# Kernel tuning notes

Measured on AMD Instinct MI355X. Metric: run time of the kernel, lower is better.

The kernel has to match this reference:

```python
import jax, jax.numpy as jnp
import numpy as np

OBS, N, IN, H = 15, 50000, 2, 64
GX, GY = 4, 4
NS = 4.0


def setup_inputs() -> dict:
    key = jax.random.key(0)
    ks = jax.random.split(key, 15)
    tgt = jax.random.uniform(ks[0], (OBS, 1, IN), minval=-2.0, maxval=2.0, dtype=jnp.float32)
    oth = jax.random.uniform(ks[1], (OBS, N, IN), minval=-3.0, maxval=3.0, dtype=jnp.float32)
    mask = jax.random.randint(ks[2], (OBS, N), 0, 2, dtype=jnp.int32)
    s = 1.0 / np.sqrt(H)
    u = lambda k, shp: jax.random.uniform(k, shp, minval=-s, maxval=s, dtype=jnp.float32)
    return dict(
        observed_trajectory_target=tgt,
        observed_trajectory_others=oth,
        neighbor_mask=mask,
        W_ih=u(ks[3], (4 * H, IN)), b_ih=u(ks[4], (4 * H,)),
        W_hh=u(ks[5], (4 * H, H)), b_hh=u(ks[6], (4 * H,)),
        W1=u(ks[7], (H, H * GX * GY)), b1=u(ks[8], (H,)),
        W2=u(ks[9], (H, H)), b2=u(ks[10], (H,)),
        Wc=u(ks[11], (2, H)), bc=u(ks[12], (2,)),
    )


def reference(observed_trajectory_target, observed_trajectory_others, neighbor_mask,
              W_ih, b_ih, W_hh, b_hh, W1, b1, W2, b2, Wc, bc):
    cw = NS / GX   # cell width
    ch = NS / GY   # cell height
    hx, hy = GX // 2, GY // 2
    half = NS / 2.0

    def lstm_cell(x, h, c):
        # torch LSTMCell: gates ordered i, f, g, o
        gates = x @ W_ih.T + b_ih + h @ W_hh.T + b_hh
        i, f, g, o = jnp.split(gates, 4, axis=-1)
        c_new = jax.nn.sigmoid(f) * c + jax.nn.sigmoid(i) * jnp.tanh(g)
        h_new = jax.nn.sigmoid(o) * jnp.tanh(c_new)
        return h_new, c_new

    def step(carry, xs):
        h_t, c_t, h_o, c_o, _ = carry
        xt, xo, m = xs                      # xt: [2], xo: [N,2], m: [N]
        ref_pos = xt[:2]
        h_t, c_t = lstm_cell(xt[None, :], h_t, c_t)
        h_o, c_o = lstm_cell(xo, h_o, c_o)
        # social grid binning (dropout is identity in eval mode)
        rel = xo[:, :2] - ref_pos           # [N,2]
        within = (jnp.abs(rel[:, 0]) <= half) & (jnp.abs(rel[:, 1]) <= half)
        cx = jnp.trunc(rel[:, 0] / cw).astype(jnp.int32) + hx  # trunc == torch .long()
        cy = jnp.trunc(rel[:, 1] / ch).astype(jnp.int32) + hy
        valid = within & (cx >= 0) & (cx < GX) & (cy >= 0) & (cy < GY) & (m != 0)
        idx = jnp.where(valid, cy * GX + cx, 0)
        contrib = jnp.where(valid[:, None], h_o, 0.0)
        social = jax.ops.segment_sum(contrib, idx, num_segments=GX * GY)  # [16,H]
        sv = social.reshape(1, -1)          # [1, 16*H]
        ctx = jax.nn.relu(sv @ W1.T + b1) @ W2.T + b2
        combined = h_t + ctx
        return (h_t, c_t, h_o, c_o, combined), None

    Nn = observed_trajectory_others.shape[1]
    init = (jnp.zeros((1, H), jnp.float32), jnp.zeros((1, H), jnp.float32),
            jnp.zeros((Nn, H), jnp.float32), jnp.zeros((Nn, H), jnp.float32),
            jnp.zeros((1, H), jnp.float32))
    xs = (observed_trajectory_target[:, 0, :], observed_trajectory_others, neighbor_mask)
    (h_t, c_t, h_o, c_o, combined), _ = jax.lax.scan(step, init, xs)
    return combined @ Wc.T + bc  # [1, 2]
```

## Files before the change

### kernel.cpp

```cpp
#include <hip/hip_runtime.h>
#include <stdint.h>

#define OBS 15
#define NTOT 50000
#define HDIM 64
#define NPB 16

typedef __attribute__((ext_vector_type(8))) short short8;
typedef __attribute__((ext_vector_type(4))) float f32x4;

static __device__ __forceinline__ unsigned short f2bf(float f) {
  unsigned u = __float_as_uint(f);
  u += 0x7fff + ((u >> 16) & 1);
  return (unsigned short)(u >> 16);
}
static __device__ __forceinline__ float bf2f(unsigned short b) {
  return __uint_as_float(((unsigned)b) << 16);
}

#if __has_builtin(__builtin_amdgcn_exp2f)
#define EXP2F(x) __builtin_amdgcn_exp2f(x)
#else
#define EXP2F(x) exp2f(x)
#endif
#if __has_builtin(__builtin_amdgcn_rcpf)
#define RCPF(x) __builtin_amdgcn_rcpf(x)
#else
#define RCPF(x) (1.0f / (x))
#endif

static __device__ __forceinline__ float sigm(float x) {
  return RCPF(1.0f + EXP2F(-1.4426950408889634f * x));
}
static __device__ __forceinline__ float tanh_(float x) {
  return 2.0f * RCPF(1.0f + EXP2F(-2.8853900817779268f * x)) - 1.0f;
}

static __device__ __forceinline__ int hidx(int r, int cb) {
  return r * 64 + ((cb ^ (r & 7)) << 3);
}

__global__ void k_zero(float* social) {
  social[threadIdx.x] = 0.0f;
}

#define MFMA_BF16 __builtin_amdgcn_mfma_f32_16x16x32_bf16

__global__ __launch_bounds__(256, 2)
void k_neigh(
    const float* __restrict__ tgt,
    const float* __restrict__ oth,
    const int* __restrict__ mask,
    const float* __restrict__ W_ih,
    const float* __restrict__ b_ih,
    const float* __restrict__ W_hh,
    const float* __restrict__ b_hh,
    float* __restrict__ social)
{
  __shared__ __align__(16) unsigned short h2[2][NPB][HDIM];
  __shared__ float xs[OBS][NPB][2];

  const int tid = threadIdx.x;
  const int l = tid & 63;
  const int w = tid >> 6;
  const int t15 = l & 15;
  const int g4 = l >> 4;
  const int n0 = blockIdx.x * NPB;

  for (int i = tid; i < OBS * NPB * 2; i += 256) {
    ((float*)xs)[i] = oth[(i >> 5) * (NTOT * 2) + n0 * 2 + (i & 31)];
  }
  for (int i = tid; i < NPB * HDIM / 2; i += 256) ((unsigned int*)h2[0])[i] = 0u;

  short8 Bhi0, Bhi1, Bhi2, Bhi3, Bhi4, Bhi5, Bhi6, Bhi7;
  short8 Blo0, Blo1, Blo2, Blo3, Blo4, Blo5, Blo6, Blo7;
  float bias2[4], wih0[4], wih1[4];
#define LOADB(q, kt, BH, BL)                                        \
  {                                                                 \
    const float* wp = &W_hh[(q * 64 + w * 16 + t15) * 64 + kt * 32 + g4 * 8]; \
    _Pragma("unroll") for (int j = 0; j < 8; ++j) {                 \
      float wv = wp[j];                                             \
      unsigned short hi = f2bf(wv);                                 \
      unsigned short lo = f2bf(wv - bf2f(hi));                      \
      BH[j] = (short)hi;                                            \
      BL[j] = (short)lo;                                            \
    }                                                               \
  }
  LOADB(0, 0, Bhi0, Blo0) LOADB(0, 1, Bhi1, Blo1)
  LOADB(1, 0, Bhi2, Blo2) LOADB(1, 1, Bhi3, Blo3)
  LOADB(2, 0, Bhi4, Blo4) LOADB(2, 1, Bhi5, Blo5)
  LOADB(3, 0, Bhi6, Blo6) LOADB(3, 1, Bhi7, Blo7)
#undef LOADB
#pragma unroll
  for (int q = 0; q < 4; ++q) {
    int g = q * 64 + w * 16 + t15;
    bias2[q] = b_ih[g] + b_hh[g];
    wih0[q] = W_ih[g * 2 + 0];
    wih1[q] = W_ih[g * 2 + 1];
  }

  f32x4 c = (f32x4){0.f, 0.f, 0.f, 0.f};
  const float refx = tgt[14 * 2 + 0];
  const float refy = tgt[14 * 2 + 1];

  __syncthreads();

  for (int t = 0; t < OBS; ++t) {
    const int cur = t & 1, nxt = cur ^ 1;
    short8 A0 = *(const short8*)&h2[cur][0][hidx(t15, g4)];
    short8 A1 = *(const short8*)&h2[cur][0][hidx(t15, 4 + g4)];

    f32x4 acc0, acc1, acc2, acc3;
#pragma unroll
    for (int r = 0; r < 4; ++r) {
      int nl = g4 * 4 + r;
      float xa = xs[t][nl][0], xb = xs[t][nl][1];
      acc0[r] = bias2[0] + xa * wih0[0] + xb * wih1[0];
      acc1[r] = bias2[1] + xa * wih0[1] + xb * wih1[1];
      acc2[r] = bias2[2] + xa * wih0[2] + xb * wih1[2];
      acc3[r] = bias2[3] + xa * wih0[3] + xb * wih1[3];
    }
    acc0 = MFMA_BF16(A0, Bhi0, acc0, 0, 0, 0);
    acc1 = MFMA_BF16(A0, Bhi2, acc1, 0, 0, 0);
    acc2 = MFMA_BF16(A0, Bhi4, acc2, 0, 0, 0);
    acc3 = MFMA_BF16(A0, Bhi6, acc3, 0, 0, 0);
    acc0 = MFMA_BF16(A1, Bhi1, acc0, 0, 0, 0);
    acc1 = MFMA_BF16(A1, Bhi3, acc1, 0, 0, 0);
    acc2 = MFMA_BF16(A1, Bhi5, acc2, 0, 0, 0);
    acc3 = MFMA_BF16(A1, Bhi7, acc3, 0, 0, 0);
    acc0 = MFMA_BF16(A0, Blo0, acc0, 0, 0, 0);
    acc1 = MFMA_BF16(A0, Blo2, acc1, 0, 0, 0);
    acc2 = MFMA_BF16(A0, Blo4, acc2, 0, 0, 0);
    acc3 = MFMA_BF16(A0, Blo6, acc3, 0, 0, 0);
    acc0 = MFMA_BF16(A1, Blo1, acc0, 0, 0, 0);
    acc1 = MFMA_BF16(A1, Blo3, acc1, 0, 0, 0);
    acc2 = MFMA_BF16(A1, Blo5, acc2, 0, 0, 0);
    acc3 = MFMA_BF16(A1, Blo7, acc3, 0, 0, 0);

    if (t < OBS - 1) {
#pragma unroll
      for (int r = 0; r < 4; ++r) {
        float si = sigm(acc0[r]);
        float sf = sigm(acc1[r]);
        float tg = tanh_(acc2[r]);
        float so = sigm(acc3[r]);
        float cn = sf * c[r] + si * tg;
        c[r] = cn;
        float h = so * tanh_(cn);
        int n = g4 * 4 + r;
        int col = w * 16 + t15;
        h2[nxt][0][hidx(n, col >> 3) + (col & 7)] = f2bf(h);
      }
      __syncthreads();
    } else {
#pragma unroll
      for (int r = 0; r < 4; ++r) {
        float si = sigm(acc0[r]);
        float sf = sigm(acc1[r]);
        float tg = tanh_(acc2[r]);
        float so = sigm(acc3[r]);
        float cn = sf * c[r] + si * tg;
        float h = so * tanh_(cn);
        int nl = g4 * 4 + r;
        int gn = n0 + nl;
        float rx = xs[OBS - 1][nl][0] - refx;
        float ry = xs[OBS - 1][nl][1] - refy;
        bool within = (fabsf(rx) <= 2.0f) && (fabsf(ry) <= 2.0f);
        int cx = (int)truncf(rx) + 2;
        int cy = (int)truncf(ry) + 2;
        bool valid = within && (cx >= 0) && (cx < 4) && (cy >= 0) && (cy < 4);
        if (valid) {
          if (mask[(OBS - 1) * NTOT + gn] != 0)
            atomicAdd(&social[(cy * 4 + cx) * HDIM + w * 16 + t15], h);
        }
      }
    }
  }
}

__global__ __launch_bounds__(512) void k_final(
    const float* __restrict__ tgt,
    const float* __restrict__ W_ih, const float* __restrict__ b_ih,
    const float* __restrict__ W_hh, const float* __restrict__ b_hh,
    const float* __restrict__ W1, const float* __restrict__ b1,
    const float* __restrict__ W2, const float* __restrict__ b2,
    const float* __restrict__ Wc, const float* __restrict__ bc,
    const float* __restrict__ social, float* __restrict__ out)
{
  __shared__ float Wt[64][256];
  __shared__ float ht[64];
  __shared__ float gp[2][256];
  __shared__ float bias2s[256];
  __shared__ float wihs[256][2];
  __shared__ float sv[1024];
  __shared__ float hid[64];
  __shared__ float comb[64];

  const int tid = threadIdx.x;
  for (int i = tid; i < 256 * 64; i += 512) {
    int g = i >> 6, k = i & 63;
    Wt[k][g] = W_hh[i];
  }
  if (tid < 256) {
    bias2s[tid] = b_ih[tid] + b_hh[tid];
    wihs[tid][0] = W_ih[tid * 2];
    wihs[tid][1] = W_ih[tid * 2 + 1];
  }
  for (int i = tid; i < 1024; i += 512) sv[i] = social[i];
  if (tid < 64) ht[tid] = 0.0f;
  float ct = 0.0f;
  __syncthreads();

  const int g = tid & 255, kh = tid >> 8;
  for (int t = 0; t < OBS; ++t) {
    float x0 = tgt[t * 2], x1 = tgt[t * 2 + 1];
    float p = 0.0f;
    int k0 = kh * 32;
#pragma unroll
    for (int k = 0; k < 32; ++k) p += ht[k0 + k] * Wt[k0 + k][g];
    gp[kh][g] = p;
    __syncthreads();
    if (tid < 64) {
      int e = tid;
      float gi = gp[0][e] + gp[1][e] + bias2s[e] + x0 * wihs[e][0] + x1 * wihs[e][1];
      float gf = gp[0][64 + e] + gp[1][64 + e] + bias2s[64 + e] + x0 * wihs[64 + e][0] + x1 * wihs[64 + e][1];
      float gg = gp[0][128 + e] + gp[1][128 + e] + bias2s[128 + e] + x0 * wihs[128 + e][0] + x1 * wihs[128 + e][1];
      float go = gp[0][192 + e] + gp[1][192 + e] + bias2s[192 + e] + x0 * wihs[192 + e][0] + x1 * wihs[192 + e][1];
      float cn = sigm(gf) * ct + sigm(gi) * tanh_(gg);
      ct = cn;
      ht[e] = sigm(go) * tanh_(cn);
    }
    __syncthreads();
  }

  const int wv = tid >> 6, ln = tid & 63;
  for (int o = wv; o < 64; o += 8) {
    float p = 0.0f;
#pragma unroll
    for (int it = 0; it < 16; ++it) {
      int j = it * 64 + ln;
      p += sv[j] * W1[o * 1024 + j];
    }
#pragma unroll
    for (int off = 32; off > 0; off >>= 1) p += __shfl_down(p, off);
    if (ln == 0) hid[o] = fmaxf(p + b1[o], 0.0f);
  }
  __syncthreads();
  for (int o = wv; o < 64; o += 8) {
    float p = hid[ln] * W2[o * 64 + ln];
#pragma unroll
    for (int off = 32; off > 0; off >>= 1) p += __shfl_down(p, off);
    if (ln == 0) comb[o] = ht[o] + p + b2[o];
  }
  __syncthreads();
  if (wv < 2) {
    float p = comb[ln] * Wc[wv * 64 + ln];
#pragma unroll
    for (int off = 32; off > 0; off >>= 1) p += __shfl_down(p, off);
    if (ln == 0) out[wv] = p + bc[wv];
  }
}

extern "C" void kernel_launch(void* const* d_in, const int* in_sizes, int n_in,
                              void* d_out, int out_size, void* d_ws, size_t ws_size,
                              hipStream_t stream) {
  const float* tgt = (const float*)d_in[0];
  const float* oth = (const float*)d_in[1];
  const int* mask = (const int*)d_in[2];
  const float* W_ih = (const float*)d_in[3];
  const float* b_ih = (const float*)d_in[4];
  const float* W_hh = (const float*)d_in[5];
  const float* b_hh = (const float*)d_in[6];
  const float* W1 = (const float*)d_in[7];
  const float* b1 = (const float*)d_in[8];
  const float* W2 = (const float*)d_in[9];
  const float* b2 = (const float*)d_in[10];
  const float* Wc = (const float*)d_in[11];
  const float* bc = (const float*)d_in[12];
  float* social = (float*)d_ws;
  float* out = (float*)d_out;

  hipLaunchKernelGGL(k_zero, dim3(1), dim3(1024), 0, stream, social);
  int nblk = NTOT / NPB;
  hipLaunchKernelGGL(k_neigh, dim3(nblk), dim3(256), 0, stream,
                     tgt, oth, mask, W_ih, b_ih, W_hh, b_hh, social);
  hipLaunchKernelGGL(k_final, dim3(1), dim3(512), 0, stream,
                     tgt, W_ih, b_ih, W_hh, b_hh, W1, b1, W2, b2, Wc, bc, social, out);
}
```

Baseline: 139.6 us.

## Swap MFMA operands, fold input projection into MFMA, move target LSTM off critical path

Each block now handles 32 neighbours instead of 16. The MFMA operands are swapped so the W_hh hi/lo split sits in the A operand and the hidden state in B. The x@W_ih + bias term is folded into an extra MFMA by packing split-bf16 inputs with a constant-one column, and hidden state is written packed with v_cvt_pk_bf16. The serial target LSTM moves from the single-block final kernel into an extra block of the neighbour kernel, so it overlaps with neighbour work and leaves the final kernel with only the MLP. The aim is to cut per-step VALU work, block count and tail latency, at the cost of more registers and possible precision loss from splitting the bias into bf16 hi/lo.

```diff
diff --git a/kernel.cpp b/kernel.cpp
--- a/kernel.cpp
+++ b/kernel.cpp
@@ -4,10 +4,14 @@
 #define OBS 15
 #define NTOT 50000
 #define HDIM 64
-#define NPB 16
+#define NPB 32
+#define NBLK_N 1563
+#define ZOFF (OBS * NPB * 8)
 
 typedef __attribute__((ext_vector_type(8))) short short8;
 typedef __attribute__((ext_vector_type(4))) float f32x4;
+typedef __attribute__((ext_vector_type(2))) unsigned int u32x2;
+typedef __attribute__((ext_vector_type(4))) unsigned int u32x4;
 
 static __device__ __forceinline__ unsigned short f2bf(float f) {
   unsigned u = __float_as_uint(f);
@@ -16,6 +20,11 @@
 }
 static __device__ __forceinline__ float bf2f(unsigned short b) {
   return __uint_as_float(((unsigned)b) << 16);
+}
+static __device__ __forceinline__ unsigned cvtpk_bf16(float lo, float hi) {
+  unsigned r;
+  asm("v_cvt_pk_bf16_f32 %0, %1, %2" : "=v"(r) : "v"(lo), "v"(hi));
+  return r;
 }
 
 #if __has_builtin(__builtin_amdgcn_exp2f)
@@ -36,10 +45,6 @@
   return 2.0f * RCPF(1.0f + EXP2F(-2.8853900817779268f * x)) - 1.0f;
 }
 
-static __device__ __forceinline__ int hidx(int r, int cb) {
-  return r * 64 + ((cb ^ (r & 7)) << 3);
-}
-
 __global__ void k_zero(float* social) {
   social[threadIdx.x] = 0.0f;
 }
@@ -55,190 +60,266 @@
     const float* __restrict__ b_ih,
     const float* __restrict__ W_hh,
     const float* __restrict__ b_hh,
-    float* __restrict__ social)
+    float* __restrict__ social,
+    float* __restrict__ ht_out)
 {
-  __shared__ __align__(16) unsigned short h2[2][NPB][HDIM];
-  __shared__ float xs[OBS][NPB][2];
+  __shared__ __align__(16) unsigned char hbuf[2][2][2048];
+  __shared__ __align__(16) unsigned short xbf[ZOFF + 8];
+  __shared__ float xs14[NPB][2];
+  __shared__ float tht[HDIM];
+  __shared__ float tgb[256];
 
   const int tid = threadIdx.x;
+
+  if (blockIdx.x == NBLK_N) {
+    const float bias = b_ih[tid] + b_hh[tid];
+    const float wi0 = W_ih[tid * 2], wi1 = W_ih[tid * 2 + 1];
+    const float4* Wr = (const float4*)&W_hh[tid * 64];
+    if (tid < HDIM) tht[tid] = 0.0f;
+    float ct = 0.0f;
+    __syncthreads();
+    for (int t = 0; t < OBS; ++t) {
+      const float x0 = tgt[t * 2], x1 = tgt[t * 2 + 1];
+      float acc = bias + x0 * wi0 + x1 * wi1;
+#pragma unroll
+      for (int k4 = 0; k4 < 16; ++k4) {
+        const float4 wv = Wr[k4];
+        const float4 hv = *(const float4*)&tht[k4 * 4];
+        acc += wv.x * hv.x + wv.y * hv.y + wv.z * hv.z + wv.w * hv.w;
+      }
+      tgb[tid] = acc;
+      __syncthreads();
+      if (tid < HDIM) {
+        const float cn =
+            sigm(tgb[64 + tid]) * ct + sigm(tgb[tid]) * tanh_(tgb[128 + tid]);
+        ct = cn;
+        tht[tid] = sigm(tgb[192 + tid]) * tanh_(cn);
+      }
+      __syncthreads();
+    }
+    if (tid < HDIM) ht_out[tid] = tht[tid];
+    return;
+  }
+
   const int l = tid & 63;
   const int w = tid >> 6;
   const int t15 = l & 15;
   const int g4 = l >> 4;
   const int n0 = blockIdx.x * NPB;
 
-  for (int i = tid; i < OBS * NPB * 2; i += 256) {
-    ((float*)xs)[i] = oth[(i >> 5) * (NTOT * 2) + n0 * 2 + (i & 31)];
-  }
-  for (int i = tid; i < NPB * HDIM / 2; i += 256) ((unsigned int*)h2[0])[i] = 0u;
-
-  short8 Bhi0, Bhi1, Bhi2, Bhi3, Bhi4, Bhi5, Bhi6, Bhi7;
-  short8 Blo0, Blo1, Blo2, Blo3, Blo4, Blo5, Blo6, Blo7;
-  float bias2[4], wih0[4], wih1[4];
-#define LOADB(q, kt, BH, BL)                                        \
-  {                                                                 \
+  for (int i = tid; i < OBS * NPB; i += 256) {
+    const int t = i >> 5, n = i & 31;
+    const int gn = n0 + n;
+    float x0 = 0.0f, x1 = 0.0f;
+    if (gn < NTOT) {
+      x0 = oth[(t * NTOT + gn) * 2 + 0];
+      x1 = oth[(t * NTOT + gn) * 2 + 1];
+    }
+    const unsigned short xh0 = f2bf(x0);
+    const unsigned short xl0 = f2bf(x0 - bf2f(xh0));
+    const unsigned short xh1 = f2bf(x1);
+    const unsigned short xl1 = f2bf(x1 - bf2f(xh1));
+    u32x4 d;
+    d.x = (unsigned)xh0 | ((unsigned)xh0 << 16);
+    d.y = (unsigned)xl0 | ((unsigned)xh1 << 16);
+    d.z = (unsigned)xh1 | ((unsigned)xl1 << 16);
+    d.w = 0x3F803F80u;
+    *(u32x4*)&xbf[i * 8] = d;
+    if (t == OBS - 1) { xs14[n][0] = x0; xs14[n][1] = x1; }
+  }
+  if (tid == 0) {
+    u32x4 zz = {0u, 0u, 0u, 0u};
+    *(u32x4*)&xbf[ZOFF] = zz;
+  }
+  for (int i = tid; i < 1024; i += 256) ((unsigned*)hbuf[0])[i] = 0u;
+
+  short8 A00, A01, A10, A11, A20, A21, A30, A31;
+  short8 L00, L01, L10, L11, L20, L21, L30, L31;
+#define LOADW(q, kt, AH, AL)                                                  \
+  {                                                                           \
     const float* wp = &W_hh[(q * 64 + w * 16 + t15) * 64 + kt * 32 + g4 * 8]; \
-    _Pragma("unroll") for (int j = 0; j < 8; ++j) {                 \
-      float wv = wp[j];                                             \
-      unsigned short hi = f2bf(wv);                                 \
-      unsigned short lo = f2bf(wv - bf2f(hi));                      \
-      BH[j] = (short)hi;                                            \
-      BL[j] = (short)lo;                                            \
-    }                                                               \
-  }
-  LOADB(0, 0, Bhi0, Blo0) LOADB(0, 1, Bhi1, Blo1)
-  LOADB(1, 0, Bhi2, Blo2) LOADB(1, 1, Bhi3, Blo3)
-  LOADB(2, 0, Bhi4, Blo4) LOADB(2, 1, Bhi5, Blo5)
-  LOADB(3, 0, Bhi6, Blo6) LOADB(3, 1, Bhi7, Blo7)
-#undef LOADB
-#pragma unroll
-  for (int q = 0; q < 4; ++q) {
-    int g = q * 64 + w * 16 + t15;
-    bias2[q] = b_ih[g] + b_hh[g];
-    wih0[q] = W_ih[g * 2 + 0];
-    wih1[q] = W_ih[g * 2 + 1];
-  }
-
-  f32x4 c = (f32x4){0.f, 0.f, 0.f, 0.f};
-  const float refx = tgt[14 * 2 + 0];
-  const float refy = tgt[14 * 2 + 1];
+    _Pragma("unroll") for (int j = 0; j < 8; ++j) {                           \
+      float wv = wp[j];                                                       \
+      unsigned short hi = f2bf(wv);                                           \
+      unsigned short lo = f2bf(wv - bf2f(hi));                                \
+      AH[j] = (short)hi;                                                      \
+      AL[j] = (short)lo;                                                      \
+    }                                                                         \
+  }
+  LOADW(0, 0, A00, L00) LOADW(0, 1, A01, L01)
+  LOADW(1, 0, A10, L10) LOADW(1, 1, A11, L11)
+  LOADW(2, 0, A20, L20) LOADW(2, 1, A21, L21)
+  LOADW(3, 0, A30, L30) LOADW(3, 1, A31, L31)
+#undef LOADW
+
+  short8 X0, X1, X2, X3;
+  {
+    u32x4 z4 = {0u, 0u, 0u, 0u};
+    X0 = X1 = X2 = X3 = __builtin_bit_cast(short8, z4);
+    if (g4 == 0) {
+#pragma unroll
+      for (int q = 0; q < 4; ++q) {
+        const int G = q * 64 + w * 16 + t15;
+        const float w0 = W_ih[G * 2 + 0], w1 = W_ih[G * 2 + 1];
+        const float bs = b_ih[G] + b_hh[G];
+        const unsigned short w0h = f2bf(w0), w0l = f2bf(w0 - bf2f(w0h));
+        const unsigned short w1h = f2bf(w1), w1l = f2bf(w1 - bf2f(w1h));
+        const unsigned short bh = f2bf(bs), bl = f2bf(bs - bf2f(bh));
+        u32x4 d;
+        d.x = (unsigned)w0h | ((unsigned)w0l << 16);
+        d.y = (unsigned)w0h | ((unsigned)w1h << 16);
+        d.z = (unsigned)w1l | ((unsigned)w1h << 16);
+        d.w = (unsigned)bh | ((unsigned)bl << 16);
+        const short8 v = __builtin_bit_cast(short8, d);
+        if (q == 0) X0 = v;
+        else if (q == 1) X1 = v;
+        else if (q == 2) X2 = v;
+        else X3 = v;
+      }
+    }
+  }
+
+  const int swz = (t15 & 7) << 4;
+  const int hr0 = t15 * 128 + ((g4 * 16) ^ swz);
+  const int hr1 = t15 * 128 + (((g4 * 16) + 64) ^ swz);
+  const int hw = t15 * 128 + (((w * 32) + (g4 * 8)) ^ swz);
+  int xo = (g4 == 0) ? (t15 * 8) : ZOFF;
+  const int xst = (g4 == 0) ? (NPB * 8) : 0;
+  const int xg1 = (g4 == 0) ? 128 : 0;
+
+  f32x4 c0 = {0.f, 0.f, 0.f, 0.f}, c1 = {0.f, 0.f, 0.f, 0.f};
+  const float refx = tgt[(OBS - 1) * 2 + 0];
+  const float refy = tgt[(OBS - 1) * 2 + 1];
 
   __syncthreads();
 
   for (int t = 0; t < OBS; ++t) {
     const int cur = t & 1, nxt = cur ^ 1;
-    short8 A0 = *(const short8*)&h2[cur][0][hidx(t15, g4)];
-    short8 A1 = *(const short8*)&h2[cur][0][hidx(t15, 4 + g4)];
-
-    f32x4 acc0, acc1, acc2, acc3;
-#pragma unroll
-    for (int r = 0; r < 4; ++r) {
-      int nl = g4 * 4 + r;
-      float xa = xs[t][nl][0], xb = xs[t][nl][1];
-      acc0[r] = bias2[0] + xa * wih0[0] + xb * wih1[0];
-      acc1[r] = bias2[1] + xa * wih0[1] + xb * wih1[1];
-      acc2[r] = bias2[2] + xa * wih0[2] + xb * wih1[2];
-      acc3[r] = bias2[3] + xa * wih0[3] + xb * wih1[3];
-    }
-    acc0 = MFMA_BF16(A0, Bhi0, acc0, 0, 0, 0);
-    acc1 = MFMA_BF16(A0, Bhi2, acc1, 0, 0, 0);
-    acc2 = MFMA_BF16(A0, Bhi4, acc2, 0, 0, 0);
-    acc3 = MFMA_BF16(A0, Bhi6, acc3, 0, 0, 0);
-    acc0 = MFMA_BF16(A1, Bhi1, acc0, 0, 0, 0);
-    acc1 = MFMA_BF16(A1, Bhi3, acc1, 0, 0, 0);
-    acc2 = MFMA_BF16(A1, Bhi5, acc2, 0, 0, 0);
-    acc3 = MFMA_BF16(A1, Bhi7, acc3, 0, 0, 0);
-    acc0 = MFMA_BF16(A0, Blo0, acc0, 0, 0, 0);
-    acc1 = MFMA_BF16(A0, Blo2, acc1, 0, 0, 0);
-    acc2 = MFMA_BF16(A0, Blo4, acc2, 0, 0, 0);
-    acc3 = MFMA_BF16(A0, Blo6, acc3, 0, 0, 0);
-    acc0 = MFMA_BF16(A1, Blo1, acc0, 0, 0, 0);
-    acc1 = MFMA_BF16(A1, Blo3, acc1, 0, 0, 0);
-    acc2 = MFMA_BF16(A1, Blo5, acc2, 0, 0, 0);
-    acc3 = MFMA_BF16(A1, Blo7, acc3, 0, 0, 0);
+    const unsigned char* hb0 = hbuf[cur][0];
+    const unsigned char* hb1 = hbuf[cur][1];
+    const short8 Bx0 = *(const short8*)&xbf[xo];
+    const short8 Bx1 = *(const short8*)&xbf[xo + xg1];
+    const short8 B00 = *(const short8*)(hb0 + hr0);
+    const short8 B01 = *(const short8*)(hb0 + hr1);
+    const short8 B10 = *(const short8*)(hb1 + hr0);
+    const short8 B11 = *(const short8*)(hb1 + hr1);
+    xo += xst;
+
+    const f32x4 z = {0.f, 0.f, 0.f, 0.f};
+    f32x4 p0 = MFMA_BF16(X0, Bx0, z, 0, 0, 0);
+    f32x4 p1 = MFMA_BF16(X1, Bx0, z, 0, 0, 0);
+    f32x4 p2 = MFMA_BF16(X2, Bx0, z, 0, 0, 0);
+    f32x4 p3 = MFMA_BF16(X3, Bx0, z, 0, 0, 0);
+    p0 = MFMA_BF16(A00, B00, p0, 0, 0, 0);
+    p1 = MFMA_BF16(A10, B00, p1, 0, 0, 0);
+    p2 = MFMA_BF16(A20, B00, p2, 0, 0, 0);
+    p3 = MFMA_BF16(A30, B00, p3, 0, 0, 0);
+    p0 = MFMA_BF16(A01, B01, p0, 0, 0, 0);
+    p1 = MFMA_BF16(A11, B01, p1, 0, 0, 0);
+    p2 = MFMA_BF16(A21, B01, p2, 0, 0, 0);
+    p3 = MFMA_BF16(A31, B01, p3, 0, 0, 0);
+    p0 = MFMA_BF16(L00, B00, p0, 0, 0, 0);
+    p1 = MFMA_BF16(L10, B00, p1, 0, 0, 0);
+    p2 = MFMA_BF16(L20, B00, p2, 0, 0, 0);
+    p3 = MFMA_BF16(L30, B00, p3, 0, 0, 0);
+    p0 = MFMA_BF16(L01, B01, p0, 0, 0, 0);
+    p1 = MFMA_BF16(L11, B01, p1, 0, 0, 0);
+    p2 = MFMA_BF16(L21, B01, p2, 0, 0, 0);
+    p3 = MFMA_BF16(L31, B01, p3, 0, 0, 0);
+    f32x4 q0 = MFMA_BF16(X0, Bx1, z, 0, 0, 0);
+    f32x4 q1 = MFMA_BF16(X1, Bx1, z, 0, 0, 0);
+    f32x4 q2 = MFMA_BF16(X2, Bx1, z, 0, 0, 0);
+    f32x4 q3 = MFMA_BF16(X3, Bx1, z, 0, 0, 0);
+    q0 = MFMA_BF16(A00, B10, q0, 0, 0, 0);
+    q1 = MFMA_BF16(A10, B10, q1, 0, 0, 0);
+    q2 = MFMA_BF16(A20, B10, q2, 0, 0, 0);
+    q3 = MFMA_BF16(A30, B10, q3, 0, 0, 0);
+    q0 = MFMA_BF16(A01, B11, q0, 0, 0, 0);
+    q1 = MFMA_BF16(A11, B11, q1, 0, 0, 0);
+    q2 = MFMA_BF16(A21, B11, q2, 0, 0, 0);
+    q3 = MFMA_BF16(A31, B11, q3, 0, 0, 0);
+    q0 = MFMA_BF16(L00, B10, q0, 0, 0, 0);
+    q1 = MFMA_BF16(L10, B10, q1, 0, 0, 0);
+    q2 = MFMA_BF16(L20, B10, q2, 0, 0, 0);
+    q3 = MFMA_BF16(L30, B10, q3, 0, 0, 0);
+    q0 = MFMA_BF16(L01, B11, q0, 0, 0, 0);
+    q1 = MFMA_BF16(L11, B11, q1, 0, 0, 0);
+    q2 = MFMA_BF16(L21, B11, q2, 0, 0, 0);
+    q3 = MFMA_BF16(L31, B11, q3, 0, 0, 0);
 
     if (t < OBS - 1) {
-#pragma unroll
-      for (int r = 0; r < 4; ++r) {
-        float si = sigm(acc0[r]);
-        float sf = sigm(acc1[r]);
-        float tg = tanh_(acc2[r]);
-        float so = sigm(acc3[r]);
-        float cn = sf * c[r] + si * tg;
-        c[r] = cn;
-        float h = so * tanh_(cn);
-        int n = g4 * 4 + r;
-        int col = w * 16 + t15;
-        h2[nxt][0][hidx(n, col >> 3) + (col & 7)] = f2bf(h);
-      }
+#define ACT(P0, P1, P2, P3, C, WB)                              \
+  {                                                             \
+    float hv[4];                                                \
+    _Pragma("unroll") for (int r = 0; r < 4; ++r) {             \
+      const float gi = P0[r], gf = P1[r], gg = P2[r],           \
+                  go = P3[r];                                   \
+      const float cn = sigm(gf) * C[r] + sigm(gi) * tanh_(gg);  \
+      C[r] = cn;                                                \
+      hv[r] = sigm(go) * tanh_(cn);                             \
+    }                                                           \
+    u32x2 pk;                                                   \
+    pk.x = cvtpk_bf16(hv[0], hv[1]);                            \
+    pk.y = cvtpk_bf16(hv[2], hv[3]);                            \
+    *(u32x2*)(WB) = pk;                                         \
+  }
+      ACT(p0, p1, p2, p3, c0, hbuf[nxt][0] + hw)
+      ACT(q0, q1, q2, q3, c1, hbuf[nxt][1] + hw)
+#undef ACT
       __syncthreads();
     } else {
-#pragma unroll
-      for (int r = 0; r < 4; ++r) {
-        float si = sigm(acc0[r]);
-        float sf = sigm(acc1[r]);
-        float tg = tanh_(acc2[r]);
-        float so = sigm(acc3[r]);
-        float cn = sf * c[r] + si * tg;
-        float h = so * tanh_(cn);
-        int nl = g4 * 4 + r;
-        int gn = n0 + nl;
-        float rx = xs[OBS - 1][nl][0] - refx;
-        float ry = xs[OBS - 1][nl][1] - refy;
-        bool within = (fabsf(rx) <= 2.0f) && (fabsf(ry) <= 2.0f);
-        int cx = (int)truncf(rx) + 2;
-        int cy = (int)truncf(ry) + 2;
-        bool valid = within && (cx >= 0) && (cx < 4) && (cy >= 0) && (cy < 4);
-        if (valid) {
-          if (mask[(OBS - 1) * NTOT + gn] != 0)
-            atomicAdd(&social[(cy * 4 + cx) * HDIM + w * 16 + t15], h);
-        }
-      }
+#define POOL(P0, P1, P2, P3, C, G)                                         \
+  {                                                                        \
+    const int nl = G * 16 + t15;                                           \
+    const int gn = n0 + nl;                                                \
+    float hv[4];                                                           \
+    _Pragma("unroll") for (int r = 0; r < 4; ++r) {                        \
+      const float gi = P0[r], gf = P1[r], gg = P2[r], go = P3[r];          \
+      const float cn = sigm(gf) * C[r] + sigm(gi) * tanh_(gg);             \
+      hv[r] = sigm(go) * tanh_(cn);                                        \
+    }                                                                      \
+    const float rx = xs14[nl][0] - refx;                                   \
+    const float ry = xs14[nl][1] - refy;                                   \
+    bool ok = (fabsf(rx) <= 2.0f) && (fabsf(ry) <= 2.0f) && (gn < NTOT);   \
+    const int cx = (int)truncf(rx) + 2;                     \
+    const int cy = (int)truncf(ry) + 2;                                    \
+    ok = ok && (cx >= 0) && (cx < 4) && (cy >= 0) && (cy < 4);             \
+    if (ok && mask[(OBS - 1) * NTOT + gn] != 0) {                          \
+      float* sp = &social[(cy * 4 + cx) * HDIM + w * 16 + g4 * 4];         \
+      _Pragma("unroll") for (int r = 0; r < 4; ++r)                        \
+        atomicAdd(&sp[r], hv[r]);                                          \
+    }                                                                      \
+  }
+      POOL(p0, p1, p2, p3, c0, 0)
+      POOL(q0, q1, q2, q3, c1, 1)
+#undef POOL
     }
   }
 }
 
 __global__ __launch_bounds__(512) void k_final(
-    const float* __restrict__ tgt,
-    const float* __restrict__ W_ih, const float* __restrict__ b_ih,
-    const float* __restrict__ W_hh, const float* __restrict__ b_hh,
     const float* __restrict__ W1, const float* __restrict__ b1,
     const float* __restrict__ W2, const float* __restrict__ b2,
     const float* __restrict__ Wc, const float* __restrict__ bc,
-    const float* __restrict__ social, float* __restrict__ out)
+    const float* __restrict__ social, const float* __restrict__ ht_g,
+    float* __restrict__ out)
 {
-  __shared__ float Wt[64][256];
-  __shared__ float ht[64];
-  __shared__ float gp[2][256];
-  __shared__ float bias2s[256];
-  __shared__ float wihs[256][2];
   __shared__ float sv[1024];
   __shared__ float hid[64];
   __shared__ float comb[64];
+  __shared__ float ht[64];
 
   const int tid = threadIdx.x;
-  for (int i = tid; i < 256 * 64; i += 512) {
-    int g = i >> 6, k = i & 63;
-    Wt[k][g] = W_hh[i];
-  }
-  if (tid < 256) {
-    bias2s[tid] = b_ih[tid] + b_hh[tid];
-    wihs[tid][0] = W_ih[tid * 2];
-    wihs[tid][1] = W_ih[tid * 2 + 1];
-  }
   for (int i = tid; i < 1024; i += 512) sv[i] = social[i];
-  if (tid < 64) ht[tid] = 0.0f;
-  float ct = 0.0f;
+  if (tid < 64) ht[tid] = ht_g[tid];
   __syncthreads();
-
-  const int g = tid & 255, kh = tid >> 8;
-  for (int t = 0; t < OBS; ++t) {
-    float x0 = tgt[t * 2], x1 = tgt[t * 2 + 1];
-    float p = 0.0f;
-    int k0 = kh * 32;
-#pragma unroll
-    for (int k = 0; k < 32; ++k) p += ht[k0 + k] * Wt[k0 + k][g];
-    gp[kh][g] = p;
-    __syncthreads();
-    if (tid < 64) {
-      int e = tid;
-      float gi = gp[0][e] + gp[1][e] + bias2s[e] + x0 * wihs[e][0] + x1 * wihs[e][1];
-      float gf = gp[0][64 + e] + gp[1][64 + e] + bias2s[64 + e] + x0 * wihs[64 + e][0] + x1 * wihs[64 + e][1];
-      float gg = gp[0][128 + e] + gp[1][128 + e] + bias2s[128 + e] + x0 * wihs[128 + e][0] + x1 * wihs[128 + e][1];
-      float go = gp[0][192 + e] + gp[1][192 + e] + bias2s[192 + e] + x0 * wihs[192 + e][0] + x1 * wihs[192 + e][1];
-      float cn = sigm(gf) * ct + sigm(gi) * tanh_(gg);
-      ct = cn;
-      ht[e] = sigm(go) * tanh_(cn);
-    }
-    __syncthreads();
-  }
 
   const int wv = tid >> 6, ln = tid & 63;
   for (int o = wv; o < 64; o += 8) {
     float p = 0.0f;
 #pragma unroll
     for (int it = 0; it < 16; ++it) {
-      int j = it * 64 + ln;
+      const int j = it * 64 + ln;
       p += sv[j] * W1[o * 1024 + j];
     }
 #pragma unroll
@@ -278,12 +359,12 @@
   const float* Wc = (const float*)d_in[11];
   const float* bc = (const float*)d_in[12];
   float* social = (float*)d_ws;
+  float* ht = social + 1024;
   float* out = (float*)d_out;
 
   hipLaunchKernelGGL(k_zero, dim3(1), dim3(1024), 0, stream, social);
-  int nblk = NTOT / NPB;
-  hipLaunchKernelGGL(k_neigh, dim3(nblk), dim3(256), 0, stream,
-                     tgt, oth, mask, W_ih, b_ih, W_hh, b_hh, social);
+  hipLaunchKernelGGL(k_neigh, dim3(NBLK_N + 1), dim3(256), 0, stream,
+                     tgt, oth, mask, W_ih, b_ih, W_hh, b_hh, social, ht);
   hipLaunchKernelGGL(k_final, dim3(1), dim3(512), 0, stream,
-                     tgt, W_ih, b_ih, W_hh, b_hh, W1, b1, W2, b2, Wc, bc, social, out);
-}
+                     W1, b1, W2, b2, Wc, bc, social, ht, out);
+}
```

Result: slower. 369.8 us (+165.0%).
